# Performance work log

Measured on AMD Instinct MI355X. Metric: run time of the kernel, lower is better.

Reference implementation:

```python
import jax, jax.numpy as jnp
import numpy as np

D = 32
H = 64
B, N, M = 2, 512, 512


def setup_inputs() -> dict:
    key = jax.random.key(0)
    ks = jax.random.split(key, 6)
    s = 0.1  # modest init scale for MLP params
    return {
        "Q": jax.random.normal(ks[0], (B, N, D), dtype=jnp.float32),
        "K": jax.random.normal(ks[1], (B, M, D), dtype=jnp.float32),
        "w1": jax.random.normal(ks[2], (D, H), dtype=jnp.float32) * s,
        "b1": jax.random.normal(ks[3], (H,), dtype=jnp.float32) * s,
        "w2": jax.random.normal(ks[4], (H, D * D), dtype=jnp.float32) * s,
        "b2": jax.random.normal(ks[5], (D * D,), dtype=jnp.float32) * s,
    }


def _cholesky_factor(x, w1, b1, w2, b2):
    """L(x) with unit-ish softplus diagonal; x: [..., D] -> L: [..., D, D]."""
    h = jax.nn.silu(x @ w1 + b1)
    raw = h @ w2 + b2                      # [..., D*D]
    raw = 5.0 * jnp.tanh(raw / 5.0)        # soft clamp
    L = (raw + jnp.eye(D, dtype=x.dtype).reshape(-1)).reshape(x.shape[:-1] + (D, D))
    tril = jnp.tril(jnp.ones((D, D), dtype=x.dtype))
    diag = jnp.eye(D, dtype=x.dtype)
    L = L * tril
    L = L * (1.0 - diag) + (jax.nn.softplus(L) + 1e-4) * diag
    return L


def reference(Q, K, w1, b1, w2, b2):
    L_q = _cholesky_factor(Q, w1, b1, w2, b2)   # [B,N,D,D]
    L_k = _cholesky_factor(K, w1, b1, w2, b2)   # [B,M,D,D]
    delta = Q[:, :, None, :] - K[:, None, :, :]  # [B,N,M,D]
    # delta^T G_avg delta = 0.5 (||L_q^T delta||^2 + ||L_k^T delta||^2)
    vq = jnp.einsum('bnij,bnmi->bnmj', L_q, delta)  # L_q^T delta
    vk = jnp.einsum('bmij,bnmi->bnmj', L_k, delta)  # L_k^T delta
    dist_sq = 0.5 * (jnp.sum(vq * vq, axis=-1) + jnp.sum(vk * vk, axis=-1))
    return jnp.sqrt(jnp.clip(dist_sq, 1e-6, 1e6))
```

## Files before the change

### kernel.cpp

```cpp
#include <hip/hip_runtime.h>
#include <math.h>

namespace {
constexpr int KF  = 1152;
constexpr int RPB = 2;
}

typedef __bf16 v8bf __attribute__((ext_vector_type(8)));
typedef float  v4f  __attribute__((ext_vector_type(4)));

__device__ __forceinline__ unsigned short f2bf(float f) {
    union { float f; unsigned u; } v; v.f = f;
    unsigned r = v.u + 0x7FFFu + ((v.u >> 16) & 1u);
    return (unsigned short)(r >> 16);
}

__device__ __forceinline__ v8bf as_v8bf(uint4 u) {
    union { uint4 u; v8bf b; } c; c.u = u; return c.b;
}

__global__ __launch_bounds__(256, 8) void k_feat(
    const float* __restrict__ Q, const float* __restrict__ K,
    const float* __restrict__ w1, const float* __restrict__ b1,
    const float* __restrict__ w2, const float* __restrict__ b2,
    unsigned short* __restrict__ featA, unsigned short* __restrict__ featB,
    float* __restrict__ cOut)
{
    __shared__ __attribute__((aligned(16))) float x_s[RPB][32];
    __shared__ __attribute__((aligned(16))) float h_s[RPB][64];
    __shared__ __attribute__((aligned(16))) float L_s[RPB][32][36];
    __shared__ __attribute__((aligned(16))) float G_s[RPB][528];
    __shared__ __attribute__((aligned(16))) float u_s[RPB][32];
    __shared__ unsigned short tri_s[528];
    __shared__ unsigned short rowoff_s[32];

    const int t  = threadIdx.x;
    const int g0 = blockIdx.x * RPB;

    for (int pr = t; pr < 528; pr += 256) {
        int j = (int)((65.0f - sqrtf(4225.0f - 8.0f * (float)pr)) * 0.5f);
        while (j > 0 && j * (65 - j) / 2 > pr) --j;
        while ((j + 1) * (64 - j) / 2 <= pr) ++j;
        int i = j + (pr - j * (65 - j) / 2);
        tri_s[pr] = (unsigned short)((i << 8) | j);
    }
    if (t < 32) rowoff_s[t] = (unsigned short)(t * (65 - t) / 2);

    if (t < RPB * 32) {
        int r = t >> 5, i = t & 31;
        int g = g0 + r;
        const float* src = (g < 1024) ? (Q + (size_t)g * 32)
                                      : (K + (size_t)(g - 1024) * 32);
        x_s[r][i] = src[i];
    }
    __syncthreads();

    if (t < RPB * 64) {
        int r = t >> 6, j = t & 63;
        float z = b1[j];
        #pragma unroll
        for (int i = 0; i < 32; ++i) z = fmaf(x_s[r][i], w1[i * 64 + j], z);
        h_s[r][j] = z / (1.0f + __expf(-z));
    }
    __syncthreads();

    {
        const int p4 = t * 4;
        const int i  = p4 >> 5;
        const int j0 = p4 & 31;
        #pragma unroll
        for (int r = 0; r < RPB; ++r) {
            float4 bq = *(const float4*)&b2[p4];
            float acc0 = bq.x, acc1 = bq.y, acc2 = bq.z, acc3 = bq.w;
            if (j0 <= i) {
                for (int jb = 0; jb < 8; ++jb) {
                    float h8[8];
                    *(float4*)&h8[0] = *(const float4*)&h_s[r][jb * 8 + 0];
                    *(float4*)&h8[4] = *(const float4*)&h_s[r][jb * 8 + 4];
                    #pragma unroll
                    for (int jj = 0; jj < 8; ++jj) {
                        float4 w = *(const float4*)&w2[(size_t)(jb * 8 + jj) * 1024 + p4];
                        acc0 = fmaf(h8[jj], w.x, acc0);
                        acc1 = fmaf(h8[jj], w.y, acc1);
                        acc2 = fmaf(h8[jj], w.z, acc2);
                        acc3 = fmaf(h8[jj], w.w, acc3);
                    }
                }
            }
            float accq[4] = { acc0, acc1, acc2, acc3 };
            float4 lv;
            float* lvp = (float*)&lv;
            #pragma unroll
            for (int e = 0; e < 4; ++e) {
                int j = j0 + e;
                float raw = accq[e];
                float ex = __expf(0.4f * raw);
                float c5 = 5.0f * (ex - 1.0f) / (ex + 1.0f);
                float val;
                if (i < j)       val = 0.0f;
                else if (i == j) { float z = c5 + 1.0f; val = log1pf(__expf(z)) + 1e-4f; }
                else             val = c5;
                lvp[e] = val;
            }
            *(float4*)&L_s[r][i][j0] = lv;
        }
    }
    __syncthreads();

    for (int idx = t; idx < RPB * 528; idx += 256) {
        int r  = idx / 528;
        int pr = idx - r * 528;
        int tv = tri_s[pr];
        int i = tv >> 8, j = tv & 255;
        const float* Li = &L_s[r][i][0];
        const float* Lj = &L_s[r][j][0];
        float s = 0.0f;
        #pragma unroll
        for (int q = 0; q < 8; ++q) {
            float4 a  = *(const float4*)&Li[q * 4];
            float4 bb = *(const float4*)&Lj[q * 4];
            s += a.x * bb.x + a.y * bb.y + a.z * bb.z + a.w * bb.w;
        }
        G_s[r][pr] = s;
    }
    __syncthreads();

    if (t < RPB * 32) {
        int r = t >> 5, i = t & 31;
        const int base_i = (int)rowoff_s[i] - i;
        float s = 0.0f;
        #pragma unroll
        for (int j = 0; j < 32; ++j) {
            int gidx = (j <= i) ? ((int)rowoff_s[j] + i - j) : (base_i + j);
            s = fmaf(G_s[r][gidx], x_s[r][j], s);
        }
        u_s[r][i] = s;
    }
    __syncthreads();

    if (t < RPB) {
        float s = 0.0f;
        #pragma unroll
        for (int i = 0; i < 32; ++i) s = fmaf(u_s[t][i], x_s[t][i], s);
        cOut[g0 + t] = s;
    }

    for (int idx = t; idx < RPB * (KF / 4); idx += 256) {
        int r   = idx / (KF / 4);
        int q   = idx - r * (KF / 4);
        int pos = q * 4;
        int g   = g0 + r;
        bool isA = (g < 1024);
        unsigned short* dst = isA ? (featA + (size_t)g * KF)
                                  : (featB + (size_t)(g - 1024) * KF);
        unsigned short ev[4];
        #pragma unroll
        for (int e = 0; e < 4; ++e) {
            int p = pos + e;
            float va;
            if (p < 1056) {
                int pr = (p < 528) ? p : p - 528;
                bool wantG = (p < 528) ? isA : !isA;
                int tv = tri_s[pr];
                int i = tv >> 8, j = tv & 255;
                float gv = G_s[r][pr] * ((i == j) ? 1.0f : 2.0f);
                float ov = x_s[r][i] * x_s[r][j];
                va = wantG ? gv : ov;
            } else if (p < 1088) {
                int i = p - 1056;
                va = isA ? u_s[r][i] : -2.0f * x_s[r][i];
            } else if (p < 1120) {
                int i = p - 1088;
                va = isA ? x_s[r][i] : -2.0f * u_s[r][i];
            } else {
                va = 0.0f;
            }
            ev[e] = f2bf(va);
        }
        uint2 w;
        w.x = (unsigned)ev[0] | ((unsigned)ev[1] << 16);
        w.y = (unsigned)ev[2] | ((unsigned)ev[3] << 16);
        *(uint2*)(dst + pos) = w;
    }
}

__global__ __launch_bounds__(256) void k_gemm(
    const unsigned short* __restrict__ featA,
    const unsigned short* __restrict__ featB,
    const float* __restrict__ cOut,
    float* __restrict__ out)
{
    __shared__ __attribute__((aligned(16))) float red[4][32][36];

    const int t    = threadIdx.x;
    const int lane = t & 63;
    const int w    = t >> 6;

    const int lin = blockIdx.x;
    const int swz = (lin & 7) * 64 + (lin >> 3);
    const int m0 = (swz & 15) * 32;
    const int n0 = ((swz >> 4) & 15) * 32;
    const int b  = swz >> 8;

    const int fr = lane & 15;
    const int fq = lane >> 4;
    const int kbase = w * 288 + fq * 8;

    const unsigned short* pA0 = featA + (size_t)(b * 512 + n0 + fr) * KF + kbase;
    const unsigned short* pA1 = pA0 + (size_t)16 * KF;
    const unsigned short* pB0 = featB + (size_t)(b * 512 + m0 + fr) * KF + kbase;
    const unsigned short* pB1 = pB0 + (size_t)16 * KF;

    v4f acc00 = {0,0,0,0}, acc01 = {0,0,0,0}, acc10 = {0,0,0,0}, acc11 = {0,0,0,0};

    uint4 bA0[4], bA1[4], bB0[4], bB1[4];
    #pragma unroll
    for (int s = 0; s < 4; ++s) {
        bA0[s] = *(const uint4*)(pA0 + s * 32);
        bA1[s] = *(const uint4*)(pA1 + s * 32);
        bB0[s] = *(const uint4*)(pB0 + s * 32);
        bB1[s] = *(const uint4*)(pB1 + s * 32);
    }

    #pragma unroll
    for (int s = 0; s < 9; ++s) {
        const int slot = s & 3;
        v8bf a0  = as_v8bf(bA0[slot]);
        v8bf a1  = as_v8bf(bA1[slot]);
        v8bf b0v = as_v8bf(bB0[slot]);
        v8bf b1v = as_v8bf(bB1[slot]);
        const int kn = s + 4;
        if (kn < 9) {
            bA0[slot] = *(const uint4*)(pA0 + kn * 32);
            bA1[slot] = *(const uint4*)(pA1 + kn * 32);
            bB0[slot] = *(const uint4*)(pB0 + kn * 32);
            bB1[slot] = *(const uint4*)(pB1 + kn * 32);
        }
        acc00 = __builtin_amdgcn_mfma_f32_16x16x32_bf16(a0, b0v, acc00, 0, 0, 0);
        acc01 = __builtin_amdgcn_mfma_f32_16x16x32_bf16(a0, b1v, acc01, 0, 0, 0);
        acc10 = __builtin_amdgcn_mfma_f32_16x16x32_bf16(a1, b0v, acc10, 0, 0, 0);
        acc11 = __builtin_amdgcn_mfma_f32_16x16x32_bf16(a1, b1v, acc11, 0, 0, 0);
    }

    #pragma unroll
    for (int v = 0; v < 4; ++v) {
        red[w][fq * 4 + v][fr]           = acc00[v];
        red[w][fq * 4 + v][fr + 16]      = acc01[v];
        red[w][16 + fq * 4 + v][fr]      = acc10[v];
        red[w][16 + fq * 4 + v][fr + 16] = acc11[v];
    }
    __syncthreads();

    const int n_l  = t >> 3;
    const int m_l0 = (t & 7) * 4;
    float4 s0 = *(const float4*)&red[0][n_l][m_l0];
    float4 s1 = *(const float4*)&red[1][n_l][m_l0];
    float4 s2 = *(const float4*)&red[2][n_l][m_l0];
    float4 s3 = *(const float4*)&red[3][n_l][m_l0];

    const int   n_g = n0 + n_l;
    const float cA  = cOut[b * 512 + n_g];
    const float4 cB = *(const float4*)&cOut[1024 + b * 512 + m0 + m_l0];

    float4 res;
    {
        float tot[4] = { s0.x + s1.x + s2.x + s3.x,
                         s0.y + s1.y + s2.y + s3.y,
                         s0.z + s1.z + s2.z + s3.z,
                         s0.w + s1.w + s2.w + s3.w };
        const float cb[4] = { cB.x, cB.y, cB.z, cB.w };
        float* rp = (float*)&res;
        #pragma unroll
        for (int e = 0; e < 4; ++e) {
            float dsq = 0.5f * (tot[e] + cA + cb[e]);
            dsq = fminf(fmaxf(dsq, 1e-6f), 1e6f);
            rp[e] = sqrtf(dsq);
        }
    }
    *(float4*)&out[((size_t)(b * 512 + n_g)) * 512 + m0 + m_l0] = res;
}

extern "C" void kernel_launch(void* const* d_in, const int* in_sizes, int n_in,
                              void* d_out, int out_size, void* d_ws, size_t ws_size,
                              hipStream_t stream)
{
    const float* Q  = (const float*)d_in[0];
    const float* K  = (const float*)d_in[1];
    const float* w1 = (const float*)d_in[2];
    const float* b1 = (const float*)d_in[3];
    const float* w2 = (const float*)d_in[4];
    const float* b2 = (const float*)d_in[5];
    float* out = (float*)d_out;

    unsigned short* featA = (unsigned short*)d_ws;
    unsigned short* featB = featA + (size_t)1024 * KF;
    float* cOut = (float*)(featB + (size_t)1024 * KF);

    k_feat<<<dim3(2048 / RPB), dim3(256), 0, stream>>>(Q, K, w1, b1, w2, b2, featA, featB, cOut);
    k_gemm<<<dim3(512), dim3(256), 0, stream>>>(featA, featB, cOut, out);
}
```

Baseline: 106.2 us.

## Map one wavefront per row in feature kernel and drop block barriers

The feature kernel now gives each 64-lane wavefront its own row, with four rows per 256-thread block. Every stage (MLP, Cholesky factor, Gram matrix, u vector, feature packing) runs wave-locally, so the block-wide __syncthreads between stages become compiler memory fences. The final dot product uses a shuffle reduction instead of a serial loop. The aim is to remove barrier stalls and idle threads between stages. The cost is a reliance on in-order LDS access within a wavefront, and each wave still streams all of w2 per row.

```diff
diff --git a/kernel.cpp b/kernel.cpp
--- a/kernel.cpp
+++ b/kernel.cpp
@@ -2,8 +2,7 @@
 #include <math.h>
 
 namespace {
-constexpr int KF  = 1152;
-constexpr int RPB = 2;
+constexpr int KF = 1152;
 }
 
 typedef __bf16 v8bf __attribute__((ext_vector_type(8)));
@@ -19,23 +18,25 @@
     union { uint4 u; v8bf b; } c; c.u = u; return c.b;
 }
 
-__global__ __launch_bounds__(256, 8) void k_feat(
+__global__ __launch_bounds__(256) void k_feat(
     const float* __restrict__ Q, const float* __restrict__ K,
     const float* __restrict__ w1, const float* __restrict__ b1,
     const float* __restrict__ w2, const float* __restrict__ b2,
     unsigned short* __restrict__ featA, unsigned short* __restrict__ featB,
     float* __restrict__ cOut)
 {
-    __shared__ __attribute__((aligned(16))) float x_s[RPB][32];
-    __shared__ __attribute__((aligned(16))) float h_s[RPB][64];
-    __shared__ __attribute__((aligned(16))) float L_s[RPB][32][36];
-    __shared__ __attribute__((aligned(16))) float G_s[RPB][528];
-    __shared__ __attribute__((aligned(16))) float u_s[RPB][32];
+    __shared__ __attribute__((aligned(16))) float x_s[4][32];
+    __shared__ __attribute__((aligned(16))) float h_s[4][64];
+    __shared__ __attribute__((aligned(16))) float L_s[4][32][36];
+    __shared__ __attribute__((aligned(16))) float G_s[4][528];
+    __shared__ __attribute__((aligned(16))) float u_s[4][32];
     __shared__ unsigned short tri_s[528];
     __shared__ unsigned short rowoff_s[32];
 
-    const int t  = threadIdx.x;
-    const int g0 = blockIdx.x * RPB;
+    const int t    = threadIdx.x;
+    const int lane = t & 63;
+    const int w    = t >> 6;
+    const int g    = blockIdx.x * 4 + w;
 
     for (int pr = t; pr < 528; pr += 256) {
         int j = (int)((65.0f - sqrtf(4225.0f - 8.0f * (float)pr)) * 0.5f);
@@ -45,142 +46,143 @@
         tri_s[pr] = (unsigned short)((i << 8) | j);
     }
     if (t < 32) rowoff_s[t] = (unsigned short)(t * (65 - t) / 2);
-
-    if (t < RPB * 32) {
-        int r = t >> 5, i = t & 31;
-        int g = g0 + r;
-        const float* src = (g < 1024) ? (Q + (size_t)g * 32)
-                                      : (K + (size_t)(g - 1024) * 32);
-        x_s[r][i] = src[i];
-    }
     __syncthreads();
 
-    if (t < RPB * 64) {
-        int r = t >> 6, j = t & 63;
+    const float* src = (g < 1024) ? (Q + (size_t)g * 32)
+                                  : (K + (size_t)(g - 1024) * 32);
+    float xi = 0.0f;
+    if (lane < 32) { xi = src[lane]; x_s[w][lane] = xi; }
+    asm volatile("" ::: "memory");
+
+    {
+        const int j = lane;
         float z = b1[j];
         #pragma unroll
-        for (int i = 0; i < 32; ++i) z = fmaf(x_s[r][i], w1[i * 64 + j], z);
-        h_s[r][j] = z / (1.0f + __expf(-z));
-    }
-    __syncthreads();
-
-    {
-        const int p4 = t * 4;
+        for (int i = 0; i < 32; ++i) z = fmaf(x_s[w][i], w1[i * 64 + j], z);
+        h_s[w][j] = z / (1.0f + __expf(-z));
+    }
+    asm volatile("" ::: "memory");
+
+    #pragma unroll
+    for (int p = 0; p < 4; ++p) {
+        const int p4 = (p * 64 + lane) * 4;
         const int i  = p4 >> 5;
         const int j0 = p4 & 31;
-        #pragma unroll
-        for (int r = 0; r < RPB; ++r) {
-            float4 bq = *(const float4*)&b2[p4];
-            float acc0 = bq.x, acc1 = bq.y, acc2 = bq.z, acc3 = bq.w;
-            if (j0 <= i) {
-                for (int jb = 0; jb < 8; ++jb) {
-                    float h8[8];
-                    *(float4*)&h8[0] = *(const float4*)&h_s[r][jb * 8 + 0];
-                    *(float4*)&h8[4] = *(const float4*)&h_s[r][jb * 8 + 4];
-                    #pragma unroll
-                    for (int jj = 0; jj < 8; ++jj) {
-                        float4 w = *(const float4*)&w2[(size_t)(jb * 8 + jj) * 1024 + p4];
-                        acc0 = fmaf(h8[jj], w.x, acc0);
-                        acc1 = fmaf(h8[jj], w.y, acc1);
-                        acc2 = fmaf(h8[jj], w.z, acc2);
-                        acc3 = fmaf(h8[jj], w.w, acc3);
-                    }
+        float4 bq = *(const float4*)&b2[p4];
+        float a0 = bq.x, a1 = bq.y, a2 = bq.z, a3 = bq.w;
+        if (j0 <= i) {
+            for (int jb = 0; jb < 8; ++jb) {
+                float h8[8];
+                *(float4*)&h8[0] = *(const float4*)&h_s[w][jb * 8 + 0];
+                *(float4*)&h8[4] = *(const float4*)&h_s[w][jb * 8 + 4];
+                #pragma unroll
+                for (int jj = 0; jj < 8; ++jj) {
+                    float4 wv4 = *(const float4*)&w2[(size_t)(jb * 8 + jj) * 1024 + p4];
+                    a0 = fmaf(h8[jj], wv4.x, a0);
+                    a1 = fmaf(h8[jj], wv4.y, a1);
+                    a2 = fmaf(h8[jj], wv4.z, a2);
+                    a3 = fmaf(h8[jj], wv4.w, a3);
                 }
             }
-            float accq[4] = { acc0, acc1, acc2, acc3 };
-            float4 lv;
-            float* lvp = (float*)&lv;
+        }
+        float accq[4] = { a0, a1, a2, a3 };
+        float4 lv;
+        float* lvp = (float*)&lv;
+        #pragma unroll
+        for (int e = 0; e < 4; ++e) {
+            int j = j0 + e;
+            float raw = accq[e];
+            float ex = __expf(0.4f * raw);
+            float c5 = 5.0f * (ex - 1.0f) / (ex + 1.0f);
+            float val;
+            if (i < j)       val = 0.0f;
+            else if (i == j) { float z = c5 + 1.0f; val = log1pf(__expf(z)) + 1e-4f; }
+            else             val = c5;
+            lvp[e] = val;
+        }
+        *(float4*)&L_s[w][i][j0] = lv;
+    }
+    asm volatile("" ::: "memory");
+
+    #pragma unroll
+    for (int pp = 0; pp < 9; ++pp) {
+        const int pr = pp * 64 + lane;
+        if (pr < 528) {
+            int tv = tri_s[pr];
+            int i = tv >> 8, j = tv & 255;
+            const float* Li = &L_s[w][i][0];
+            const float* Lj = &L_s[w][j][0];
+            float s = 0.0f;
             #pragma unroll
-            for (int e = 0; e < 4; ++e) {
-                int j = j0 + e;
-                float raw = accq[e];
-                float ex = __expf(0.4f * raw);
-                float c5 = 5.0f * (ex - 1.0f) / (ex + 1.0f);
-                float val;
-                if (i < j)       val = 0.0f;
-                else if (i == j) { float z = c5 + 1.0f; val = log1pf(__expf(z)) + 1e-4f; }
-                else             val = c5;
-                lvp[e] = val;
+            for (int q = 0; q < 8; ++q) {
+                float4 a  = *(const float4*)&Li[q * 4];
+                float4 bb = *(const float4*)&Lj[q * 4];
+                s += a.x * bb.x + a.y * bb.y + a.z * bb.z + a.w * bb.w;
             }
-            *(float4*)&L_s[r][i][j0] = lv;
-        }
-    }
-    __syncthreads();
-
-    for (int idx = t; idx < RPB * 528; idx += 256) {
-        int r  = idx / 528;
-        int pr = idx - r * 528;
-        int tv = tri_s[pr];
-        int i = tv >> 8, j = tv & 255;
-        const float* Li = &L_s[r][i][0];
-        const float* Lj = &L_s[r][j][0];
-        float s = 0.0f;
-        #pragma unroll
-        for (int q = 0; q < 8; ++q) {
-            float4 a  = *(const float4*)&Li[q * 4];
-            float4 bb = *(const float4*)&Lj[q * 4];
-            s += a.x * bb.x + a.y * bb.y + a.z * bb.z + a.w * bb.w;
-        }
-        G_s[r][pr] = s;
-    }
-    __syncthreads();
-
-    if (t < RPB * 32) {
-        int r = t >> 5, i = t & 31;
+            G_s[w][pr] = s;
+        }
+    }
+    asm volatile("" ::: "memory");
+
+    float uval = 0.0f;
+    if (lane < 32) {
+        const int i = lane;
         const int base_i = (int)rowoff_s[i] - i;
-        float s = 0.0f;
         #pragma unroll
         for (int j = 0; j < 32; ++j) {
             int gidx = (j <= i) ? ((int)rowoff_s[j] + i - j) : (base_i + j);
-            s = fmaf(G_s[r][gidx], x_s[r][j], s);
-        }
-        u_s[r][i] = s;
-    }
-    __syncthreads();
-
-    if (t < RPB) {
-        float s = 0.0f;
-        #pragma unroll
-        for (int i = 0; i < 32; ++i) s = fmaf(u_s[t][i], x_s[t][i], s);
-        cOut[g0 + t] = s;
-    }
-
-    for (int idx = t; idx < RPB * (KF / 4); idx += 256) {
-        int r   = idx / (KF / 4);
-        int q   = idx - r * (KF / 4);
-        int pos = q * 4;
-        int g   = g0 + r;
-        bool isA = (g < 1024);
+            uval = fmaf(G_s[w][gidx], x_s[w][j], uval);
+        }
+        u_s[w][i] = uval;
+    }
+    asm volatile("" ::: "memory");
+
+    {
+        float prod = (lane < 32) ? uval * xi : 0.0f;
+        #pragma unroll
+        for (int off = 16; off > 0; off >>= 1) prod += __shfl_down(prod, off);
+        if (lane == 0) cOut[g] = prod;
+    }
+
+    {
+        const bool isA = (g < 1024);
         unsigned short* dst = isA ? (featA + (size_t)g * KF)
                                   : (featB + (size_t)(g - 1024) * KF);
-        unsigned short ev[4];
-        #pragma unroll
-        for (int e = 0; e < 4; ++e) {
-            int p = pos + e;
-            float va;
-            if (p < 1056) {
-                int pr = (p < 528) ? p : p - 528;
-                bool wantG = (p < 528) ? isA : !isA;
-                int tv = tri_s[pr];
-                int i = tv >> 8, j = tv & 255;
-                float gv = G_s[r][pr] * ((i == j) ? 1.0f : 2.0f);
-                float ov = x_s[r][i] * x_s[r][j];
-                va = wantG ? gv : ov;
-            } else if (p < 1088) {
-                int i = p - 1056;
-                va = isA ? u_s[r][i] : -2.0f * x_s[r][i];
-            } else if (p < 1120) {
-                int i = p - 1088;
-                va = isA ? x_s[r][i] : -2.0f * u_s[r][i];
-            } else {
-                va = 0.0f;
+        #pragma unroll
+        for (int pp = 0; pp < 5; ++pp) {
+            const int qidx = pp * 64 + lane;
+            if (qidx < KF / 4) {
+                const int pos = qidx * 4;
+                unsigned short ev[4];
+                #pragma unroll
+                for (int e = 0; e < 4; ++e) {
+                    int p = pos + e;
+                    float va;
+                    if (p < 1056) {
+                        int pr = (p < 528) ? p : p - 528;
+                        bool wantG = (p < 528) ? isA : !isA;
+                        int tv = tri_s[pr];
+                        int i = tv >> 8, j = tv & 255;
+                        float gv = G_s[w][pr] * ((i == j) ? 1.0f : 2.0f);
+                        float ov = x_s[w][i] * x_s[w][j];
+                        va = wantG ? gv : ov;
+                    } else if (p < 1088) {
+                        int i = p - 1056;
+                        va = isA ? u_s[w][i] : -2.0f * x_s[w][i];
+                    } else if (p < 1120) {
+                        int i = p - 1088;
+                        va = isA ? x_s[w][i] : -2.0f * u_s[w][i];
+                    } else {
+                        va = 0.0f;
+                    }
+                    ev[e] = f2bf(va);
+                }
+                uint2 wpk;
+                wpk.x = (unsigned)ev[0] | ((unsigned)ev[1] << 16);
+                wpk.y = (unsigned)ev[2] | ((unsigned)ev[3] << 16);
+                *(uint2*)(dst + pos) = wpk;
             }
-            ev[e] = f2bf(va);
-        }
-        uint2 w;
-        w.x = (unsigned)ev[0] | ((unsigned)ev[1] << 16);
-        w.y = (unsigned)ev[2] | ((unsigned)ev[3] << 16);
-        *(uint2*)(dst + pos) = w;
+        }
     }
 }
 
@@ -296,6 +298,6 @@
     unsigned short* featB = featA + (size_t)1024 * KF;
     float* cOut = (float*)(featB + (size_t)1024 * KF);
 
-    k_feat<<<dim3(2048 / RPB), dim3(256), 0, stream>>>(Q, K, w1, b1, w2, b2, featA, featB, cOut);
+    k_feat<<<dim3(512), dim3(256), 0, stream>>>(Q, K, w1, b1, w2, b2, featA, featB, cOut);
     k_gemm<<<dim3(512), dim3(256), 0, stream>>>(featA, featB, cOut, out);
 }
```

Result: slower. 112.3 us (+5.8%).
